# Performance work log

Hardware: AMD Instinct MI355X
Metric: run time of the kernel (lower is better)

## Reference

```python
import jax, jax.numpy as jnp
import numpy as np

N = 4096
HIDDEN = 256
NUM_HEADS = 8
HEAD_DIM = HIDDEN // NUM_HEADS
LN_EPS = 1e-3


def setup_inputs() -> dict:
    key = jax.random.key(0)
    ks = jax.random.split(key, 8)
    s = 1.0 / np.sqrt(HIDDEN)
    feat = jax.random.normal(ks[0], (N, HIDDEN), dtype=jnp.float32)
    Wq = jax.random.normal(ks[1], (HIDDEN, HIDDEN), dtype=jnp.float32) * s
    bq = jnp.zeros((HIDDEN,), dtype=jnp.float32)
    Wkv = jax.random.normal(ks[2], (HIDDEN, 2 * HIDDEN), dtype=jnp.float32) * s
    bkv = jnp.zeros((2 * HIDDEN,), dtype=jnp.float32)
    Weg = jax.random.normal(ks[3], (HIDDEN, 2 * NUM_HEADS), dtype=jnp.float32) * s
    beg = jnp.zeros((2 * NUM_HEADS,), dtype=jnp.float32)
    ln_g = jnp.ones((HIDDEN,), dtype=jnp.float32)
    ln_b = jnp.zeros((HIDDEN,), dtype=jnp.float32)
    return {"feat": feat, "Wq": Wq, "bq": bq, "Wkv": Wkv, "bkv": bkv,
            "Weg": Weg, "beg": beg, "ln_g": ln_g, "ln_b": ln_b}


def reference(feat, Wq, bq, Wkv, bkv, Weg, beg, ln_g, ln_b):
    n = feat.shape[0]
    # projections
    Q = feat @ Wq + bq                                  # [N, hidden]
    KV = feat @ Wkv + bkv                               # [N, 2*hidden]
    K, V = jnp.split(KV, 2, axis=-1)
    EG = feat @ Weg + beg                               # [N, 2*heads]
    E, G = jnp.split(EG, 2, axis=-1)                    # each [N, heads]
    # reshape to [N, head_dim, heads] (heads is the FAST axis, as in torch .view)
    Q = Q.reshape(n, HEAD_DIM, NUM_HEADS) * (HEAD_DIM ** -0.5)
    K = K.reshape(n, HEAD_DIM, NUM_HEADS)
    V = V.reshape(n, HEAD_DIM, NUM_HEADS)
    # all-pairs scores with per-j edge bias: [N, N, heads]
    H = jnp.einsum('idh,jdh->ijh', Q, K) + E[None, :, :]
    # softmax over i (axis 0), post-softmax sigmoid gate (per j, h)
    A = jax.nn.softmax(H, axis=0) * jax.nn.sigmoid(G)[None, :, :]
    Va = jnp.einsum('ijh,jdh->idh', A, V).reshape(n, HIDDEN)
    # layernorm eps=1e-3
    mu = jnp.mean(Va, axis=-1, keepdims=True)
    var = jnp.var(Va, axis=-1, keepdims=True)
    return (Va - mu) * jax.lax.rsqrt(var + LN_EPS) * ln_g + ln_b
```

## Files before the change

### kernel.cpp

```cpp
#include <hip/hip_runtime.h>
#include <hip/hip_bf16.h>

#define N 4096
#define HID 256
#define NH 8
#define HD 32
#define NC 784
#define CH 16
#define JSPAN (N / CH)

typedef __attribute__((ext_vector_type(8))) short short8;
typedef __attribute__((ext_vector_type(4))) short short4v;
typedef __attribute__((ext_vector_type(4))) float f32x4;
typedef __attribute__((ext_vector_type(2))) unsigned int uint2v;
typedef __attribute__((ext_vector_type(4))) unsigned int uint4v;

#define QSCALE 0.25503482f

static __device__ __forceinline__ unsigned short f2bf(float f) {
    union { float f; unsigned u; } v; v.f = f;
    unsigned r = v.u + 0x7fff + ((v.u >> 16) & 1);
    return (unsigned short)(r >> 16);
}
static __device__ __forceinline__ float bf2f(unsigned short u) {
    union { unsigned u; float f; } v; v.u = ((unsigned)u) << 16; return v.f;
}
static __device__ __forceinline__ unsigned packhu(float a, float b) {
    unsigned ua = __builtin_bit_cast(unsigned, a) + 0x8000u;
    unsigned ub = __builtin_bit_cast(unsigned, b) + 0x8000u;
    return __builtin_amdgcn_perm(ub, ua, 0x07060302u);
}

__global__ void k_prep(const float* __restrict__ feat, const float* __restrict__ Wq,
                       const float* __restrict__ Wkv, const float* __restrict__ Weg,
                       const float* __restrict__ bq, const float* __restrict__ bkv,
                       const float* __restrict__ beg, unsigned short* __restrict__ featb,
                       unsigned short* __restrict__ WbT, float* __restrict__ bC,
                       float* __restrict__ colS) {
    int bx = blockIdx.x;
    if (bx < 1024) {
        int t = bx * 256 + threadIdx.x;
        float4 v = ((const float4*)feat)[t];
        short4v o;
        o[0] = (short)f2bf(v.x); o[1] = (short)f2bf(v.y);
        o[2] = (short)f2bf(v.z); o[3] = (short)f2bf(v.w);
        ((short4v*)featb)[t] = o;
    } else {
        int c = bx - 1024, k = threadIdx.x;
        float w, b;
        if (c < 256)      { w = Wq[k * 256 + c];          b = bq[c]; }
        else if (c < 768) { w = Wkv[k * 512 + (c - 256)]; b = bkv[c - 256]; }
        else              { w = Weg[k * 16 + (c - 768)];  b = beg[c - 768]; }
        WbT[c * 256 + k] = f2bf(w);
        if (k == 0) bC[c] = b;
        if (c < 128) colS[c * 256 + k] = 0.f;
    }
}

__global__ __launch_bounds__(256) void k_proj(const unsigned short* __restrict__ featb,
                                              const unsigned short* __restrict__ WbT,
                                              const float* __restrict__ bC,
                                              unsigned short* __restrict__ Qp,
                                              unsigned short* __restrict__ Kp,
                                              unsigned short* __restrict__ VpT,
                                              float* __restrict__ sigG) {
    int w = threadIdx.x >> 6, l = threadIdx.x & 63;
    int il = l & 15, g = l >> 4;
    int c0 = blockIdx.x * 16;
    int i0 = (blockIdx.y * 4 + w) * 16;
    const short8* Arow = (const short8*)(featb + (size_t)(i0 + il) * HID);
    const short8* Brow = (const short8*)(WbT + (size_t)(c0 + il) * HID);
    f32x4 acc = {0.f, 0.f, 0.f, 0.f};
#pragma unroll
    for (int k0 = 0; k0 < HID; k0 += 32) {
        short8 a = Arow[(k0 >> 3) + g];
        short8 b = Brow[(k0 >> 3) + g];
        acc = __builtin_amdgcn_mfma_f32_16x16x32_bf16(a, b, acc, 0, 0, 0);
    }
    int c = c0 + il;
    float bias = bC[c];
#pragma unroll
    for (int r = 0; r < 4; ++r) {
        int i = i0 + g * 4 + r;
        float val = acc[r] + bias;
        if (c < 256) {
            int h = c & 7, d = c >> 3;
            Qp[((size_t)h * N + i) * HD + d] = f2bf(val * QSCALE);
        } else if (c < 512) {
            int cc = c - 256, h = cc & 7, d = cc >> 3;
            Kp[((size_t)h * N + i) * HD + d] = f2bf(val);
        } else if (c < 768) {
            int cc = c - 512, h = cc & 7, d = cc >> 3;
            VpT[((size_t)h * HD + d) * N + i] = f2bf(val);
        } else {
            int cc = c - 768;
            if (cc >= 8) sigG[(size_t)(cc - 8) * N + i] = 1.f / (1.f + __expf(-val));
        }
    }
}

__global__ __launch_bounds__(256) void k_pass1(const unsigned short* __restrict__ Qp,
                                               const unsigned short* __restrict__ Kp,
                                               float* __restrict__ colS) {
    int w = threadIdx.x >> 6, l = threadIdx.x & 63;
    int il = l & 15, g = l >> 4;
    int h = blockIdx.y;
    int j0 = (blockIdx.x * 4 + w) * 64;
    const unsigned short* Kh = Kp + (size_t)h * N * HD;
    short8 Kf[4];
#pragma unroll
    for (int t = 0; t < 4; ++t)
        Kf[t] = *(const short8*)(Kh + (size_t)(j0 + 16 * t + il) * HD + g * 8);
    const unsigned short* Qh = Qp + (size_t)h * N * HD;
    f32x4 z = {0.f, 0.f, 0.f, 0.f};
    float s[4] = {0.f, 0.f, 0.f, 0.f};
    int ibeg = blockIdx.z * 128;
    short8 Qa0 = *(const short8*)(Qh + (size_t)(ibeg + il) * HD + g * 8);
    short8 Qb0 = *(const short8*)(Qh + (size_t)(ibeg + 16 + il) * HD + g * 8);
    short8 Qa1 = *(const short8*)(Qh + (size_t)(ibeg + 32 + il) * HD + g * 8);
    short8 Qb1 = *(const short8*)(Qh + (size_t)(ibeg + 48 + il) * HD + g * 8);
#pragma unroll
    for (int it = 0; it < 4; ++it) {
        int i0 = ibeg + it * 32;
        short8 cQa = Qa0, cQb = Qb0;
        Qa0 = Qa1; Qb0 = Qb1;
        int in = i0 + 64;
        Qa1 = *(const short8*)(Qh + (size_t)(in + il) * HD + g * 8);
        Qb1 = *(const short8*)(Qh + (size_t)(in + 16 + il) * HD + g * 8);
        __builtin_amdgcn_sched_barrier(0);
#pragma unroll
        for (int t = 0; t < 4; ++t) {
            f32x4 Sa = __builtin_amdgcn_mfma_f32_16x16x32_bf16(cQa, Kf[t], z, 0, 0, 0);
            f32x4 Sb = __builtin_amdgcn_mfma_f32_16x16x32_bf16(cQb, Kf[t], z, 0, 0, 0);
            s[t] += ((__builtin_amdgcn_exp2f(Sa[0]) + __builtin_amdgcn_exp2f(Sa[1]))
                   + (__builtin_amdgcn_exp2f(Sa[2]) + __builtin_amdgcn_exp2f(Sa[3])))
                  + ((__builtin_amdgcn_exp2f(Sb[0]) + __builtin_amdgcn_exp2f(Sb[1]))
                   + (__builtin_amdgcn_exp2f(Sb[2]) + __builtin_amdgcn_exp2f(Sb[3])));
        }
    }
#pragma unroll
    for (int t = 0; t < 4; ++t) {
        s[t] += __shfl_xor(s[t], 16);
        s[t] += __shfl_xor(s[t], 32);
    }
    if (g == 0) {
#pragma unroll
        for (int t = 0; t < 4; ++t)
            atomicAdd(&colS[(size_t)h * N + j0 + 16 * t + il], s[t]);
    }
}

__global__ void k_vprep(unsigned short* __restrict__ VpT,
                        const float* __restrict__ sigG,
                        const float* __restrict__ colS) {
    int row = blockIdx.x >> 1;
    int j0 = ((blockIdx.x & 1) * 256 + threadIdx.x) * 8;
    int h = row >> 5;
    unsigned short* p = VpT + (size_t)row * N + j0;
    short8 v = *(short8*)p;
    const float* sg = sigG + (size_t)h * N + j0;
    const float* cs = colS + (size_t)h * N + j0;
    float sc[8];
#pragma unroll
    for (int k = 0; k < 8; ++k)
        sc[k] = sg[k] * __builtin_amdgcn_rcpf(cs[k]);
    uint4v ov;
    ov[0] = packhu(bf2f((unsigned short)v[0]) * sc[0], bf2f((unsigned short)v[1]) * sc[1]);
    ov[1] = packhu(bf2f((unsigned short)v[2]) * sc[2], bf2f((unsigned short)v[3]) * sc[3]);
    ov[2] = packhu(bf2f((unsigned short)v[4]) * sc[4], bf2f((unsigned short)v[5]) * sc[5]);
    ov[3] = packhu(bf2f((unsigned short)v[6]) * sc[6], bf2f((unsigned short)v[7]) * sc[7]);
    *(uint4v*)p = ov;
}

static __device__ __forceinline__ short8 frag_dance(f32x4 Sa, f32x4 Sb) {
    unsigned A0 = packhu(__builtin_amdgcn_exp2f(Sa[0]), __builtin_amdgcn_exp2f(Sa[1]));
    unsigned A1 = packhu(__builtin_amdgcn_exp2f(Sa[2]), __builtin_amdgcn_exp2f(Sa[3]));
    unsigned B0 = packhu(__builtin_amdgcn_exp2f(Sb[0]), __builtin_amdgcn_exp2f(Sb[1]));
    unsigned B1 = packhu(__builtin_amdgcn_exp2f(Sb[2]), __builtin_amdgcn_exp2f(Sb[3]));
    uint2v r1 = __builtin_amdgcn_permlane32_swap(A0, B0, false, false);
    uint2v r2 = __builtin_amdgcn_permlane16_swap(r1[0], r1[1], false, false);
    uint2v r3 = __builtin_amdgcn_permlane32_swap(A1, B1, false, false);
    uint2v r4 = __builtin_amdgcn_permlane16_swap(r3[0], r3[1], false, false);
    uint4v pu;
    pu[0] = r2[0]; pu[1] = r4[0]; pu[2] = r2[1]; pu[3] = r4[1];
    return __builtin_bit_cast(short8, pu);
}

__global__ __launch_bounds__(128) void k_pass2(const unsigned short* __restrict__ Qp,
                                               const unsigned short* __restrict__ Kp,
                                               const unsigned short* __restrict__ VpT,
                                               unsigned short* __restrict__ Vpb) {
    int w = threadIdx.x >> 6, l = threadIdx.x & 63;
    int il = l & 15, g = l >> 4;
    int h = blockIdx.y;
    int i0 = blockIdx.x * 256 + w * 128;
    int jbeg = blockIdx.z * JSPAN;
    const unsigned short* Qh = Qp + (size_t)h * N * HD;
    const unsigned short* Kh = Kp + ((size_t)h * N + jbeg) * HD;
    const unsigned short* Vh = VpT + (size_t)h * HD * N + jbeg;
    short8 Qf[8];
#pragma unroll
    for (int q = 0; q < 8; ++q)
        Qf[q] = *(const short8*)(Qh + (size_t)(i0 + q * 16 + il) * HD + g * 8);
    f32x4 z = {0.f, 0.f, 0.f, 0.f};
    f32x4 acc[8][2];
#pragma unroll
    for (int q = 0; q < 8; ++q) { acc[q][0] = z; acc[q][1] = z; }
    short8 K0 = *(const short8*)(Kh + (size_t)il * HD + g * 8);
    short8 K1 = *(const short8*)(Kh + (size_t)(16 + il) * HD + g * 8);
    short8 V0 = *(const short8*)(Vh + (size_t)il * N + g * 8);
    short8 V1 = *(const short8*)(Vh + (size_t)(16 + il) * N + g * 8);
#pragma unroll
    for (int it = 0; it < 8; ++it) {
        int jb = it * 32;
        short8 cK0 = K0, cK1 = K1, cV0 = V0, cV1 = V1;
        int jn = jb + 32;
        K0 = *(const short8*)(Kh + (size_t)(jn + il) * HD + g * 8);
        K1 = *(const short8*)(Kh + (size_t)(jn + 16 + il) * HD + g * 8);
        V0 = *(const short8*)(Vh + (size_t)il * N + jn + g * 8);
        V1 = *(const short8*)(Vh + (size_t)(16 + il) * N + jn + g * 8);
        __builtin_amdgcn_sched_barrier(0);
        __builtin_amdgcn_s_setprio(1);
#pragma unroll
        for (int q = 0; q < 8; ++q) {
            f32x4 SA = __builtin_amdgcn_mfma_f32_16x16x32_bf16(cK0, Qf[q], z, 0, 0, 0);
            f32x4 SB = __builtin_amdgcn_mfma_f32_16x16x32_bf16(cK1, Qf[q], z, 0, 0, 0);
            short8 Pa = frag_dance(SA, SB);
            acc[q][0] = __builtin_amdgcn_mfma_f32_16x16x32_bf16(Pa, cV0, acc[q][0], 0, 0, 0);
            acc[q][1] = __builtin_amdgcn_mfma_f32_16x16x32_bf16(Pa, cV1, acc[q][1], 0, 0, 0);
        }
        __builtin_amdgcn_s_setprio(0);
    }
    unsigned short* Vout = Vpb + (size_t)(blockIdx.z * NH + h) * N * HD;
#pragma unroll
    for (int q = 0; q < 8; ++q) {
#pragma unroll
        for (int r = 0; r < 4; ++r) {
            int ia = i0 + q * 16 + g * 4 + r;
            Vout[(size_t)ia * HD + il]      = f2bf(acc[q][0][r]);
            Vout[(size_t)ia * HD + 16 + il] = f2bf(acc[q][1][r]);
        }
    }
}

__global__ __launch_bounds__(256) void k_ln(const unsigned short* __restrict__ Vpb,
                                            const float* __restrict__ gam,
                                            const float* __restrict__ bet,
                                            float* __restrict__ out) {
    int w = threadIdx.x >> 6, l = threadIdx.x & 63;
    int i = blockIdx.x * 4 + w;
    int h = l >> 3, d0 = (l & 7) << 2;
    f32x4 x = {0.f, 0.f, 0.f, 0.f};
#pragma unroll
    for (int c = 0; c < CH; ++c) {
        short4v v = *(const short4v*)(Vpb + ((size_t)(c * NH + h) * N + i) * HD + d0);
        x[0] += bf2f((unsigned short)v[0]); x[1] += bf2f((unsigned short)v[1]);
        x[2] += bf2f((unsigned short)v[2]); x[3] += bf2f((unsigned short)v[3]);
    }
    float s1 = x[0] + x[1] + x[2] + x[3];
    float s2 = x[0] * x[0] + x[1] * x[1] + x[2] * x[2] + x[3] * x[3];
#pragma unroll
    for (int off = 1; off < 64; off <<= 1) {
        s1 += __shfl_xor(s1, off);
        s2 += __shfl_xor(s2, off);
    }
    float mu = s1 * (1.f / 256.f);
    float var = s2 * (1.f / 256.f) - mu * mu;
    float rs = rsqrtf(var + 1e-3f);
#pragma unroll
    for (int r = 0; r < 4; ++r) {
        int c = (d0 + r) * 8 + h;
        out[(size_t)i * HID + c] = (x[r] - mu) * rs * gam[c] + bet[c];
    }
}

extern "C" void kernel_launch(void* const* d_in, const int* in_sizes, int n_in,
                              void* d_out, int out_size, void* d_ws, size_t ws_size,
                              hipStream_t stream) {
    const float* feat = (const float*)d_in[0];
    const float* Wq   = (const float*)d_in[1];
    const float* bq   = (const float*)d_in[2];
    const float* Wkv  = (const float*)d_in[3];
    const float* bkv  = (const float*)d_in[4];
    const float* Weg  = (const float*)d_in[5];
    const float* beg  = (const float*)d_in[6];
    const float* ln_g = (const float*)d_in[7];
    const float* ln_b = (const float*)d_in[8];
    float* out = (float*)d_out;

    char* ws = (char*)d_ws;
    unsigned short* Qp    = (unsigned short*)(ws + 0);
    unsigned short* Kp    = (unsigned short*)(ws + (2u << 20));
    unsigned short* VpT   = (unsigned short*)(ws + (4u << 20));
    unsigned short* featb = (unsigned short*)(ws + (6u << 20));
    unsigned short* WbT   = (unsigned short*)(ws + (8u << 20));
    float* bC   = (float*)(ws + (8u << 20) + (512u << 10));
    float* sigG = (float*)(ws + (8u << 20) + (528u << 10));
    float* colS = (float*)(ws + (8u << 20) + (656u << 10));
    unsigned short* Vpb = (unsigned short*)(ws + (9u << 20));

    k_prep<<<dim3(1024 + NC), 256, 0, stream>>>(feat, Wq, Wkv, Weg, bq, bkv, beg,
                                                featb, WbT, bC, colS);
    k_proj<<<dim3(49, 64), 256, 0, stream>>>(featb, WbT, bC, Qp, Kp, VpT, sigG);
    k_pass1<<<dim3(16, NH, 32), 256, 0, stream>>>(Qp, Kp, colS);
    k_vprep<<<dim3(512), 256, 0, stream>>>(VpT, sigG, colS);
    k_pass2<<<dim3(16, NH, CH), 128, 0, stream>>>(Qp, Kp, VpT, Vpb);
    k_ln<<<dim3(1024), 256, 0, stream>>>(Vpb, ln_g, ln_b, out);
}
```

Measured before the change: 99.27 us.

## Stage K/V tiles in LDS via async global_load_lds, double-buffered, 4 waves per block

The k_pass2 kernel now loads each K/V tile once per block into LDS with direct global-to-LDS loads, using a double buffer and an XOR swizzle. Previously every wave fetched the same K/V fragments from global memory into registers on its own. The block grows from 2 to 4 waves, each handling 64 rows instead of 128, which raises occupancy and spreads K/V reuse across more waves. In exchange it adds a __syncthreads per iteration and gives each wave half as much MFMA work per K/V tile.

```diff
diff --git a/kernel.cpp b/kernel.cpp
--- a/kernel.cpp
+++ b/kernel.cpp
@@ -16,6 +16,10 @@
 typedef __attribute__((ext_vector_type(4))) unsigned int uint4v;
 
 #define QSCALE 0.25503482f
+
+#define GLOAD(gp, sp) __builtin_amdgcn_global_load_lds( \
+    (const __attribute__((address_space(1))) unsigned int*)(gp), \
+    (__attribute__((address_space(3))) unsigned int*)(sp), 16, 0, 0)
 
 static __device__ __forceinline__ unsigned short f2bf(float f) {
     union { float f; unsigned u; } v; v.f = f;
@@ -186,43 +190,56 @@
     return __builtin_bit_cast(short8, pu);
 }
 
-__global__ __launch_bounds__(128) void k_pass2(const unsigned short* __restrict__ Qp,
+__global__ __launch_bounds__(256) void k_pass2(const unsigned short* __restrict__ Qp,
                                                const unsigned short* __restrict__ Kp,
                                                const unsigned short* __restrict__ VpT,
                                                unsigned short* __restrict__ Vpb) {
+    __shared__ __align__(16) char smem[2][4096];
     int w = threadIdx.x >> 6, l = threadIdx.x & 63;
     int il = l & 15, g = l >> 4;
     int h = blockIdx.y;
-    int i0 = blockIdx.x * 256 + w * 128;
+    int i0 = blockIdx.x * 256 + w * 64;
     int jbeg = blockIdx.z * JSPAN;
     const unsigned short* Qh = Qp + (size_t)h * N * HD;
-    const unsigned short* Kh = Kp + ((size_t)h * N + jbeg) * HD;
-    const unsigned short* Vh = VpT + (size_t)h * HD * N + jbeg;
-    short8 Qf[8];
-#pragma unroll
-    for (int q = 0; q < 8; ++q)
+    const char* Khc = (const char*)(Kp + ((size_t)h * N + jbeg) * HD);
+    const char* Vhc = (const char*)(VpT + (size_t)h * HD * N + jbeg);
+    const char* gsrc;
+    int gstep;
+    {
+        int s = (w & 1) * 64 + l;
+        int r = s >> 2, c = s & 3;
+        int cs = c ^ ((r + (r >> 2)) & 3);
+        if (w < 2) { gsrc = Khc + r * 64 + cs * 16;           gstep = 2048; }
+        else       { gsrc = Vhc + (size_t)r * 8192 + cs * 16; gstep = 64;  }
+    }
+    char* lq0 = smem[0] + w * 1024;
+    char* lq1 = smem[1] + w * 1024;
+    int fo = il * 64 + ((g ^ ((il + (il >> 2)) & 3)) << 4);
+    short8 Qf[4];
+#pragma unroll
+    for (int q = 0; q < 4; ++q)
         Qf[q] = *(const short8*)(Qh + (size_t)(i0 + q * 16 + il) * HD + g * 8);
     f32x4 z = {0.f, 0.f, 0.f, 0.f};
-    f32x4 acc[8][2];
-#pragma unroll
-    for (int q = 0; q < 8; ++q) { acc[q][0] = z; acc[q][1] = z; }
-    short8 K0 = *(const short8*)(Kh + (size_t)il * HD + g * 8);
-    short8 K1 = *(const short8*)(Kh + (size_t)(16 + il) * HD + g * 8);
-    short8 V0 = *(const short8*)(Vh + (size_t)il * N + g * 8);
-    short8 V1 = *(const short8*)(Vh + (size_t)(16 + il) * N + g * 8);
+    f32x4 acc[4][2];
+#pragma unroll
+    for (int q = 0; q < 4; ++q) { acc[q][0] = z; acc[q][1] = z; }
+    GLOAD(gsrc, lq0);
+    gsrc += gstep;
+    __syncthreads();
 #pragma unroll
     for (int it = 0; it < 8; ++it) {
-        int jb = it * 32;
-        short8 cK0 = K0, cK1 = K1, cV0 = V0, cV1 = V1;
-        int jn = jb + 32;
-        K0 = *(const short8*)(Kh + (size_t)(jn + il) * HD + g * 8);
-        K1 = *(const short8*)(Kh + (size_t)(jn + 16 + il) * HD + g * 8);
-        V0 = *(const short8*)(Vh + (size_t)il * N + jn + g * 8);
-        V1 = *(const short8*)(Vh + (size_t)(16 + il) * N + jn + g * 8);
+        int b = it & 1;
+        GLOAD(gsrc, b ? lq0 : lq1);
+        gsrc += gstep;
         __builtin_amdgcn_sched_barrier(0);
+        const char* kb = smem[b];
+        short8 cK0 = *(const short8*)(kb + fo);
+        short8 cK1 = *(const short8*)(kb + 1024 + fo);
+        short8 cV0 = *(const short8*)(kb + 2048 + fo);
+        short8 cV1 = *(const short8*)(kb + 3072 + fo);
         __builtin_amdgcn_s_setprio(1);
 #pragma unroll
-        for (int q = 0; q < 8; ++q) {
+        for (int q = 0; q < 4; ++q) {
             f32x4 SA = __builtin_amdgcn_mfma_f32_16x16x32_bf16(cK0, Qf[q], z, 0, 0, 0);
             f32x4 SB = __builtin_amdgcn_mfma_f32_16x16x32_bf16(cK1, Qf[q], z, 0, 0, 0);
             short8 Pa = frag_dance(SA, SB);
@@ -230,10 +247,11 @@
             acc[q][1] = __builtin_amdgcn_mfma_f32_16x16x32_bf16(Pa, cV1, acc[q][1], 0, 0, 0);
         }
         __builtin_amdgcn_s_setprio(0);
+        __syncthreads();
     }
     unsigned short* Vout = Vpb + (size_t)(blockIdx.z * NH + h) * N * HD;
 #pragma unroll
-    for (int q = 0; q < 8; ++q) {
+    for (int q = 0; q < 4; ++q) {
 #pragma unroll
         for (int r = 0; r < 4; ++r) {
             int ia = i0 + q * 16 + g * 4 + r;
@@ -304,6 +322,6 @@
     k_proj<<<dim3(49, 64), 256, 0, stream>>>(featb, WbT, bC, Qp, Kp, VpT, sigG);
     k_pass1<<<dim3(16, NH, 32), 256, 0, stream>>>(Qp, Kp, colS);
     k_vprep<<<dim3(512), 256, 0, stream>>>(VpT, sigG, colS);
-    k_pass2<<<dim3(16, NH, CH), 128, 0, stream>>>(Qp, Kp, VpT, Vpb);
+    k_pass2<<<dim3(16, NH, CH), 256, 0, stream>>>(Qp, Kp, VpT, Vpb);
     k_ln<<<dim3(1024), 256, 0, stream>>>(Vpb, ln_g, ln_b, out);
 }
```

Result: no change. 97.56 us (median of 2 runs) (-1.7%).
